# Optimization experiments

Hardware: AMD Instinct MI355X
Metric: run time of the kernel (lower is better)

## Reference

```python
import jax, jax.numpy as jnp
import numpy as np

N = 100000
E = 1600000
D_IN = 128
D_H = 128
D_OUT = 128
LN_EPS = 1e-5
NORM_EPS = 1e-12


def _sage_conv(x, src, dst, Wl, bl, Wr):
    # PyG SAGEConv(mean): out = lin_l(mean_{j in N(i)} x_j) + lin_r(x_i)
    msgs = x[src]                                             # [E, d] gather
    summed = jax.ops.segment_sum(msgs, dst, num_segments=N)   # [N, d]
    cnt = jax.ops.segment_sum(jnp.ones((src.shape[0],), x.dtype), dst, num_segments=N)
    mean = summed / jnp.maximum(cnt, 1.0)[:, None]
    return mean @ Wl + bl + x @ Wr


def _layer_norm(x, g, b):
    mu = jnp.mean(x, axis=-1, keepdims=True)
    var = jnp.mean(jnp.square(x - mu), axis=-1, keepdims=True)
    return (x - mu) * jax.lax.rsqrt(var + LN_EPS) * g + b


def setup_inputs() -> dict:
    key = jax.random.key(0)
    ks = jax.random.split(key, 20)
    x = jax.random.normal(ks[0], (N, D_IN), dtype=jnp.float32)
    edge_index = jax.random.randint(ks[1], (2, E), 0, N, dtype=jnp.int64)
    dims = [(D_IN, D_H), (D_H, D_H), (D_H, D_OUT)]
    inp = {"x": x, "edge_index": edge_index}
    for i, (di, do) in enumerate(dims):
        s = 1.0 / np.sqrt(di)
        inp[f"Wl{i}"] = jax.random.normal(ks[2 + 5 * i], (di, do), dtype=jnp.float32) * s
        inp[f"bl{i}"] = jnp.zeros((do,), dtype=jnp.float32)
        inp[f"Wr{i}"] = jax.random.normal(ks[3 + 5 * i], (di, do), dtype=jnp.float32) * s
        inp[f"g{i}"] = jnp.ones((do,), dtype=jnp.float32)
        inp[f"b{i}"] = jnp.zeros((do,), dtype=jnp.float32)
    return inp


def reference(x, edge_index, Wl0, bl0, Wr0, g0, b0, Wl1, bl1, Wr1, g1, b1, Wl2, bl2, Wr2, g2, b2):
    src, dst = edge_index[0], edge_index[1]
    params = [(Wl0, bl0, Wr0, g0, b0), (Wl1, bl1, Wr1, g1, b1), (Wl2, bl2, Wr2, g2, b2)]
    h = x
    for i, (Wl, bl, Wr, g, b) in enumerate(params):
        h = _sage_conv(h, src, dst, Wl, bl, Wr)
        h = _layer_norm(h, g, b)
        if i < len(params) - 1:
            h = jax.nn.elu(h)
            # dropout is identity in eval mode
    # F.normalize(p=2, dim=-1)
    nrm = jnp.sqrt(jnp.sum(jnp.square(h), axis=-1, keepdims=True))
    return h / jnp.maximum(nrm, NORM_EPS)
```

## Files before the change

kernel.cpp:

```cpp
#include <hip/hip_runtime.h>
#include <hip/hip_bf16.h>
#include <math.h>

#define N_NODES 100000
#define N_EDGES 1600000
#define D 128
#define NB 391
#define BSTRIDE 6000

#define OFF_SSRC 0
#define OFF_OFFS 6400000
#define OFF_PACK 6800016
#define OFF_GC   7193232
#define OFF_BB   7195296
#define OFF_M    7204112
#define OFF_XHI  58404112
#define OFF_XLO  84004112

typedef __attribute__((ext_vector_type(8))) short short8;
typedef __attribute__((ext_vector_type(4))) float floatx4;

__device__ __forceinline__ unsigned short f2bf(float f) {
    unsigned int u = __float_as_uint(f);
    u += 0x7fffu + ((u >> 16) & 1u);
    return (unsigned short)(u >> 16);
}
__device__ __forceinline__ float bf2f(unsigned short h) {
    return __uint_as_float(((unsigned int)h) << 16);
}

__global__ __launch_bounds__(256) void part_kernel(const int* __restrict__ src,
                                                   const int* __restrict__ dst,
                                                   int* __restrict__ gcur,
                                                   uint2* __restrict__ staging) {
    __shared__ int hist[NB];
    __shared__ int base[NB];
    int t = threadIdx.x;
    int e0 = blockIdx.x * 4096;
    for (int i = t; i < NB; i += 256) hist[i] = 0;
    __syncthreads();
    int d[16];
#pragma unroll
    for (int i = 0; i < 16; ++i) {
        int e = e0 + i * 256 + t;
        d[i] = (e < N_EDGES) ? dst[e] : -1;
        if (d[i] >= 0) atomicAdd(&hist[d[i] >> 8], 1);
    }
    __syncthreads();
    for (int i = t; i < NB; i += 256) {
        int h = hist[i];
        base[i] = h ? atomicAdd(&gcur[i], h) : 0;
    }
    __syncthreads();
    for (int i = t; i < NB; i += 256) hist[i] = 0;
    __syncthreads();
#pragma unroll
    for (int i = 0; i < 16; ++i) {
        if (d[i] >= 0) {
            int e = e0 + i * 256 + t;
            int b = d[i] >> 8;
            int slot = atomicAdd(&hist[b], 1);
            staging[b * BSTRIDE + base[b] + slot] =
                make_uint2((unsigned)src[e], (unsigned)(d[i] & 255));
        }
    }
}

__global__ void bscan_kernel(const int* __restrict__ gcur, int* __restrict__ bbase,
                             int* __restrict__ offs) {
    __shared__ int sh[512];
    int t = threadIdx.x;
    int v = (t < NB) ? gcur[t] : 0;
    sh[t] = v;
    __syncthreads();
    for (int off = 1; off < 512; off <<= 1) {
        int y = (t >= off) ? sh[t - off] : 0;
        __syncthreads();
        sh[t] += y;
        __syncthreads();
    }
    if (t < NB) bbase[t] = sh[t] - v;
    if (t == 0) offs[N_NODES] = N_EDGES;
}

__global__ __launch_bounds__(256) void bsort_kernel(const uint2* __restrict__ staging,
                                                    const int* __restrict__ gcur,
                                                    const int* __restrict__ bbase,
                                                    int* __restrict__ offs,
                                                    int* __restrict__ s_src) {
    __shared__ int cnt[256];
    __shared__ int scn[256];
    __shared__ int ssrc[BSTRIDE];
    int b = blockIdx.x;
    int t = threadIdx.x;
    int n = gcur[b];
    int base_out = bbase[b];
    cnt[t] = 0;
    __syncthreads();
    for (int e = t; e < n; e += 256) {
        uint2 v = staging[b * BSTRIDE + e];
        atomicAdd(&cnt[v.y], 1);
    }
    __syncthreads();
    int v = cnt[t];
    scn[t] = v;
    __syncthreads();
    for (int off = 1; off < 256; off <<= 1) {
        int y = (t >= off) ? scn[t - off] : 0;
        __syncthreads();
        scn[t] += y;
        __syncthreads();
    }
    int ex = scn[t] - v;
    int node = b * 256 + t;
    if (node < N_NODES) offs[node] = base_out + ex;
    cnt[t] = ex;
    __syncthreads();
    for (int e = t; e < n; e += 256) {
        uint2 w = staging[b * BSTRIDE + e];
        int slot = atomicAdd(&cnt[w.y], 1);
        ssrc[slot] = (int)w.x;
    }
    __syncthreads();
    for (int e = t; e < n; e += 256) s_src[base_out + e] = ssrc[e];
}

__global__ void pack_kernel(const float* __restrict__ Wl0, const float* __restrict__ Wr0,
                            const float* __restrict__ Wl1, const float* __restrict__ Wr1,
                            const float* __restrict__ Wl2, const float* __restrict__ Wr2,
                            unsigned short* __restrict__ pack) {
    int tid = blockIdx.x * blockDim.x + threadIdx.x;
    int l = tid >> 15;
    int r = tid & 32767;
    int k = r >> 7;
    int n = r & 127;
    const float* Wl = (l == 0) ? Wl0 : (l == 1) ? Wl1 : Wl2;
    const float* Wr = (l == 0) ? Wr0 : (l == 1) ? Wr1 : Wr2;
    float v = (k < 128) ? Wl[k * 128 + n] : Wr[(k - 128) * 128 + n];
    unsigned short hi = f2bf(v);
    unsigned short lo = f2bf(v - bf2f(hi));
    int ct = n >> 4, ks = k >> 5, lane = ((k >> 3) & 3) * 16 + (n & 15), j = k & 7;
    int idx = ((ct * 8 + ks) * 64 + lane) * 8 + j;
    pack[l * 65536 + idx] = hi;
    pack[l * 65536 + 32768 + idx] = lo;
}

__global__ __launch_bounds__(256) void cvt_kernel(const float* __restrict__ x,
                                                  unsigned int* __restrict__ Xhi,
                                                  unsigned int* __restrict__ Xlo) {
    int i = blockIdx.x * 256 + threadIdx.x;
    float2 v = ((const float2*)x)[i];
    unsigned short h0 = f2bf(v.x), h1 = f2bf(v.y);
    unsigned short l0 = f2bf(v.x - bf2f(h0)), l1 = f2bf(v.y - bf2f(h1));
    Xhi[i] = (unsigned int)h0 | ((unsigned int)h1 << 16);
    Xlo[i] = (unsigned int)l0 | ((unsigned int)l1 << 16);
}

__global__ __launch_bounds__(256, 5) void fused_kernel(const uint4* __restrict__ X4,
                                                       const unsigned short* __restrict__ Xh,
                                                       const unsigned short* __restrict__ Xl,
                                                       unsigned short* __restrict__ XhO,
                                                       unsigned short* __restrict__ XlO,
                                                       const int* __restrict__ s_src,
                                                       const int* __restrict__ offs,
                                                       const unsigned short* __restrict__ packh,
                                                       const unsigned short* __restrict__ packl,
                                                       const float* __restrict__ bl,
                                                       const float* __restrict__ g,
                                                       const float* __restrict__ b,
                                                       float* __restrict__ outf, int last) {
    __shared__ float lmean[64 * 128];
    int t = threadIdx.x;
    int wid = t >> 6, lane = t & 63;
    int sub = lane >> 4, li = lane & 15;
    int nodebase = blockIdx.x * 64;

    int off_l = offs[min(nodebase + wid * 16 + min(lane, 16), N_NODES)];

#define ACC_U4(u)                                                                  \
    do {                                                                           \
        const unsigned int w_[4] = {(u).x, (u).y, (u).z, (u).w};                   \
        _Pragma("unroll") for (int j_ = 0; j_ < 4; ++j_) {                         \
            acc[2 * j_]     += bf2f((unsigned short)w_[j_]);                       \
            acc[2 * j_ + 1] += bf2f((unsigned short)(w_[j_] >> 16));               \
        }                                                                          \
    } while (0)

    for (int i = 0; i < 16; ++i) {
        int lrow = wid * 16 + i;
        int beg = __shfl(off_l, i);
        int end = __shfl(off_l, i + 1);
        int deg = end - beg;
        float acc[8];
#pragma unroll
        for (int j = 0; j < 8; ++j) acc[j] = 0.f;

        for (int cbase = 0; cbase < deg; cbase += 64) {
            int cnt = min(deg - cbase, 64);
            int myidx = s_src[min(beg + cbase + lane, N_EDGES - 1)];
            int j = 0;
            for (; j + 16 <= cnt; j += 16) {
                int i0 = __shfl(myidx, j + sub);
                int i1 = __shfl(myidx, j + 4 + sub);
                int i2 = __shfl(myidx, j + 8 + sub);
                int i3 = __shfl(myidx, j + 12 + sub);
                uint4 u0 = X4[i0 * 16 + li];
                uint4 u1 = X4[i1 * 16 + li];
                uint4 u2 = X4[i2 * 16 + li];
                uint4 u3 = X4[i3 * 16 + li];
                ACC_U4(u0); ACC_U4(u1); ACC_U4(u2); ACC_U4(u3);
            }
            if (j + 8 <= cnt) {
                int i0 = __shfl(myidx, j + sub);
                int i1 = __shfl(myidx, j + 4 + sub);
                uint4 u0 = X4[i0 * 16 + li];
                uint4 u1 = X4[i1 * 16 + li];
                ACC_U4(u0); ACC_U4(u1);
                j += 8;
            }
            if (j + 4 <= cnt) {
                int i0 = __shfl(myidx, j + sub);
                uint4 u0 = X4[i0 * 16 + li];
                ACC_U4(u0);
                j += 4;
            }
            int rem = cnt - j;
            if (rem > 0) {
                int i0 = __shfl(myidx, j + min(sub, rem - 1));
                uint4 u0 = X4[i0 * 16 + li];
                if (sub < rem) ACC_U4(u0);
            }
        }
#pragma unroll
        for (int j = 0; j < 8; ++j) {
            acc[j] += __shfl_xor(acc[j], 16);
            acc[j] += __shfl_xor(acc[j], 32);
        }
        float inv = 1.0f / fmaxf((float)deg, 1.0f);
        if (sub < 2) {
            int chunk = li * 2 + sub;
            floatx4 v = {acc[sub * 4] * inv, acc[sub * 4 + 1] * inv,
                         acc[sub * 4 + 2] * inv, acc[sub * 4 + 3] * inv};
            *(floatx4*)&lmean[lrow * 128 + ((chunk ^ (lrow & 7)) << 2)] = v;
        }
    }
#undef ACC_U4

    int colb = lane & 15;
    int quad = lane >> 4;
    int kq = quad * 8;
    int tilebase = nodebase + wid * 16;

    int rowA = min(tilebase + colb, N_NODES - 1);
    int lrowA = wid * 16 + colb;
    int rsalt = lrowA & 7;

    floatx4 acc[8];
#pragma unroll
    for (int ct = 0; ct < 8; ++ct) acc[ct] = (floatx4){0.f, 0.f, 0.f, 0.f};

#pragma unroll
    for (int ks = 0; ks < 4; ++ks) {
        int chunk0 = ks * 8 + quad * 2;
        short8 ah, al;
        {
            floatx4 v0 = *(const floatx4*)&lmean[lrowA * 128 + ((chunk0 ^ rsalt) << 2)];
            floatx4 v1 = *(const floatx4*)&lmean[lrowA * 128 + (((chunk0 + 1) ^ rsalt) << 2)];
            float v[8] = {v0[0], v0[1], v0[2], v0[3], v1[0], v1[1], v1[2], v1[3]};
#pragma unroll
            for (int j = 0; j < 8; ++j) {
                unsigned short hi = f2bf(v[j]);
                ah[j] = (short)hi;
                al[j] = (short)f2bf(v[j] - bf2f(hi));
            }
        }
#pragma unroll
        for (int ct = 0; ct < 8; ++ct) {
            int fo = ((ct * 8 + ks) << 9) + (lane << 3);
            short8 bh = *(const short8*)(packh + fo);
            short8 bo = *(const short8*)(packl + fo);
            acc[ct] = __builtin_amdgcn_mfma_f32_16x16x32_bf16(ah, bh, acc[ct], 0, 0, 0);
            acc[ct] = __builtin_amdgcn_mfma_f32_16x16x32_bf16(al, bh, acc[ct], 0, 0, 0);
            acc[ct] = __builtin_amdgcn_mfma_f32_16x16x32_bf16(ah, bo, acc[ct], 0, 0, 0);
        }
    }
#pragma unroll
    for (int ks = 4; ks < 8; ++ks) {
        int kof = (ks - 4) * 32 + kq;
        long o = (long)rowA * D + kof;
        short8 ah = *(const short8*)(Xh + o);
        short8 al = *(const short8*)(Xl + o);
#pragma unroll
        for (int ct = 0; ct < 8; ++ct) {
            int fo = ((ct * 8 + ks) << 9) + (lane << 3);
            short8 bh = *(const short8*)(packh + fo);
            short8 bo = *(const short8*)(packl + fo);
            acc[ct] = __builtin_amdgcn_mfma_f32_16x16x32_bf16(ah, bh, acc[ct], 0, 0, 0);
            acc[ct] = __builtin_amdgcn_mfma_f32_16x16x32_bf16(al, bh, acc[ct], 0, 0, 0);
            acc[ct] = __builtin_amdgcn_mfma_f32_16x16x32_bf16(ah, bo, acc[ct], 0, 0, 0);
        }
    }

    float bb[8], gg[8], b2[8];
#pragma unroll
    for (int ct = 0; ct < 8; ++ct) {
        bb[ct] = bl[ct * 16 + colb];
        gg[ct] = g[ct * 16 + colb];
        b2[ct] = b[ct * 16 + colb];
    }

#pragma unroll
    for (int ct = 0; ct < 8; ++ct)
#pragma unroll
        for (int e = 0; e < 4; ++e) acc[ct][e] += bb[ct];
    float mu[4], rstd[4];
#pragma unroll
    for (int e = 0; e < 4; ++e) {
        float s = 0.f;
#pragma unroll
        for (int ct = 0; ct < 8; ++ct) s += acc[ct][e];
        s += __shfl_xor(s, 1); s += __shfl_xor(s, 2);
        s += __shfl_xor(s, 4); s += __shfl_xor(s, 8);
        mu[e] = s * (1.0f / 128.0f);
    }
#pragma unroll
    for (int e = 0; e < 4; ++e) {
        float q = 0.f;
#pragma unroll
        for (int ct = 0; ct < 8; ++ct) {
            float d = acc[ct][e] - mu[e];
            q += d * d;
        }
        q += __shfl_xor(q, 1); q += __shfl_xor(q, 2);
        q += __shfl_xor(q, 4); q += __shfl_xor(q, 8);
        rstd[e] = rsqrtf(q * (1.0f / 128.0f) + 1e-5f);
    }
#pragma unroll
    for (int ct = 0; ct < 8; ++ct)
#pragma unroll
        for (int e = 0; e < 4; ++e) {
            float y = (acc[ct][e] - mu[e]) * rstd[e] * gg[ct] + b2[ct];
            if (!last) y = (y > 0.f) ? y : expm1f(y);
            acc[ct][e] = y;
        }
    if (last) {
#pragma unroll
        for (int e = 0; e < 4; ++e) {
            float ss = 0.f;
#pragma unroll
            for (int ct = 0; ct < 8; ++ct) {
                float y = acc[ct][e];
                ss += y * y;
            }
            ss += __shfl_xor(ss, 1); ss += __shfl_xor(ss, 2);
            ss += __shfl_xor(ss, 4); ss += __shfl_xor(ss, 8);
            float inv = 1.0f / fmaxf(sqrtf(ss), 1e-12f);
#pragma unroll
            for (int ct = 0; ct < 8; ++ct) acc[ct][e] *= inv;
        }
#pragma unroll
        for (int e = 0; e < 4; ++e) {
            int row = tilebase + quad * 4 + e;
            if (row < N_NODES) {
#pragma unroll
                for (int ct = 0; ct < 8; ++ct)
                    outf[(long)row * D + ct * 16 + colb] = acc[ct][e];
            }
        }
    } else {
#pragma unroll
        for (int e = 0; e < 4; ++e) {
            int row = tilebase + quad * 4 + e;
            if (row < N_NODES) {
#pragma unroll
                for (int ct = 0; ct < 8; ++ct) {
                    float y = acc[ct][e];
                    unsigned short hh = f2bf(y);
                    unsigned short ll = f2bf(y - bf2f(hh));
                    long o = (long)row * D + ct * 16 + colb;
                    XhO[o] = hh;
                    XlO[o] = ll;
                }
            }
        }
    }
}

extern "C" void kernel_launch(void* const* d_in, const int* in_sizes, int n_in,
                              void* d_out, int out_size, void* d_ws, size_t ws_size,
                              hipStream_t stream) {
    const float* x = (const float*)d_in[0];
    const int* edges = (const int*)d_in[1];
    const int* src = edges;
    const int* dst = edges + N_EDGES;
    const float* Wl[3] = {(const float*)d_in[2], (const float*)d_in[7],  (const float*)d_in[12]};
    const float* bl[3] = {(const float*)d_in[3], (const float*)d_in[8],  (const float*)d_in[13]};
    const float* Wr[3] = {(const float*)d_in[4], (const float*)d_in[9],  (const float*)d_in[14]};
    const float* g[3]  = {(const float*)d_in[5], (const float*)d_in[10], (const float*)d_in[15]};
    const float* b[3]  = {(const float*)d_in[6], (const float*)d_in[11], (const float*)d_in[16]};

    char* ws = (char*)d_ws;
    int* s_src = (int*)(ws + OFF_SSRC);
    int* offs  = (int*)(ws + OFF_OFFS);
    unsigned short* wpack = (unsigned short*)(ws + OFF_PACK);
    int* gcur  = (int*)(ws + OFF_GC);
    int* bbase = (int*)(ws + OFF_BB);
    uint2* staging = (uint2*)(ws + OFF_M);
    unsigned short* XhB = (unsigned short*)(ws + OFF_M);
    unsigned short* XlB = (unsigned short*)(ws + OFF_M + 25600000);
    unsigned short* XhA = (unsigned short*)(ws + OFF_XHI);
    unsigned short* XlA = (unsigned short*)(ws + OFF_XLO);
    float* out = (float*)d_out;

    hipMemsetAsync(gcur, 0, NB * sizeof(int), stream);
    part_kernel<<<(N_EDGES + 4095) / 4096, 256, 0, stream>>>(src, dst, gcur, staging);
    bscan_kernel<<<1, 512, 0, stream>>>(gcur, bbase, offs);
    bsort_kernel<<<NB, 256, 0, stream>>>(staging, gcur, bbase, offs, s_src);
    pack_kernel<<<(3 * 32768) / 256, 256, 0, stream>>>(Wl[0], Wr[0], Wl[1], Wr[1], Wl[2], Wr[2], wpack);
    cvt_kernel<<<(N_NODES * 64) / 256, 256, 0, stream>>>(x, (unsigned int*)XhA, (unsigned int*)XlA);

    const int FB = (N_NODES + 63) / 64;
    unsigned short* ph[3] = {wpack, wpack + 65536, wpack + 131072};

    fused_kernel<<<FB, 256, 0, stream>>>((const uint4*)XhA, XhA, XlA, XhB, XlB,
                                         s_src, offs, ph[0], ph[0] + 32768,
                                         bl[0], g[0], b[0], nullptr, 0);
    fused_kernel<<<FB, 256, 0, stream>>>((const uint4*)XhB, XhB, XlB, XhA, XlA,
                                         s_src, offs, ph[1], ph[1] + 32768,
                                         bl[1], g[1], b[1], nullptr, 0);
    fused_kernel<<<FB, 256, 0, stream>>>((const uint4*)XhA, XhA, XlA, nullptr, nullptr,
                                         s_src, offs, ph[2], ph[2] + 32768,
                                         bl[2], g[2], b[2], out, 1);
}
```

Baseline: 592.0 us.

## Replace bucketed two-pass CSR build with global-atomic degree count and scatter

Swaps the bucket partition plus per-bucket LDS sort for a plain CSR build: global atomic degree histogram, three-stage prefix scan, then a global-atomic scatter of source indices. The degree histogram is fused into the x-to-bf16 split conversion kernel so one launch does both. It drops the staging buffer and the capacity-limited BSTRIDE buckets but relies on heavy global atomics. Neighbor order within a node becomes nondeterministic, which can change float summation order.

```diff
diff --git a/kernel.cpp b/kernel.cpp
--- a/kernel.cpp
+++ b/kernel.cpp
@@ -6,7 +6,6 @@
 #define N_EDGES 1600000
 #define D 128
 #define NB 391
-#define BSTRIDE 6000
 
 #define OFF_SSRC 0
 #define OFF_OFFS 6400000
@@ -29,48 +28,45 @@
     return __uint_as_float(((unsigned int)h) << 16);
 }
 
-__global__ __launch_bounds__(256) void part_kernel(const int* __restrict__ src,
-                                                   const int* __restrict__ dst,
-                                                   int* __restrict__ gcur,
-                                                   uint2* __restrict__ staging) {
-    __shared__ int hist[NB];
-    __shared__ int base[NB];
-    int t = threadIdx.x;
-    int e0 = blockIdx.x * 4096;
-    for (int i = t; i < NB; i += 256) hist[i] = 0;
+__global__ __launch_bounds__(256) void cvt_hist_kernel(const float* __restrict__ x,
+                                                       unsigned int* __restrict__ Xhi,
+                                                       unsigned int* __restrict__ Xlo,
+                                                       const int* __restrict__ dst,
+                                                       int* __restrict__ deg) {
+    int bid = blockIdx.x, t = threadIdx.x;
+    if (t < 64) atomicAdd(&deg[dst[bid * 64 + t]], 1);
+    int i = bid * 256 + t;
+    float2 v = ((const float2*)x)[i];
+    unsigned short h0 = f2bf(v.x), h1 = f2bf(v.y);
+    unsigned short l0 = f2bf(v.x - bf2f(h0)), l1 = f2bf(v.y - bf2f(h1));
+    Xhi[i] = (unsigned int)h0 | ((unsigned int)h1 << 16);
+    Xlo[i] = (unsigned int)l0 | ((unsigned int)l1 << 16);
+}
+
+__global__ __launch_bounds__(256) void scan1_kernel(const int* __restrict__ deg,
+                                                    int* __restrict__ offs,
+                                                    int* __restrict__ aux) {
+    __shared__ int sh[256];
+    int b = blockIdx.x, t = threadIdx.x;
+    int node = b * 256 + t;
+    int v = (node < N_NODES) ? deg[node] : 0;
+    sh[t] = v;
     __syncthreads();
-    int d[16];
-#pragma unroll
-    for (int i = 0; i < 16; ++i) {
-        int e = e0 + i * 256 + t;
-        d[i] = (e < N_EDGES) ? dst[e] : -1;
-        if (d[i] >= 0) atomicAdd(&hist[d[i] >> 8], 1);
-    }
-    __syncthreads();
-    for (int i = t; i < NB; i += 256) {
-        int h = hist[i];
-        base[i] = h ? atomicAdd(&gcur[i], h) : 0;
-    }
-    __syncthreads();
-    for (int i = t; i < NB; i += 256) hist[i] = 0;
-    __syncthreads();
-#pragma unroll
-    for (int i = 0; i < 16; ++i) {
-        if (d[i] >= 0) {
-            int e = e0 + i * 256 + t;
-            int b = d[i] >> 8;
-            int slot = atomicAdd(&hist[b], 1);
-            staging[b * BSTRIDE + base[b] + slot] =
-                make_uint2((unsigned)src[e], (unsigned)(d[i] & 255));
-        }
-    }
-}
-
-__global__ void bscan_kernel(const int* __restrict__ gcur, int* __restrict__ bbase,
+    for (int off = 1; off < 256; off <<= 1) {
+        int y = (t >= off) ? sh[t - off] : 0;
+        __syncthreads();
+        sh[t] += y;
+        __syncthreads();
+    }
+    if (node < N_NODES) offs[node] = sh[t] - v;
+    if (t == 255) aux[b] = sh[255];
+}
+
+__global__ void bscan_kernel(const int* __restrict__ aux, int* __restrict__ bbase,
                              int* __restrict__ offs) {
     __shared__ int sh[512];
     int t = threadIdx.x;
-    int v = (t < NB) ? gcur[t] : 0;
+    int v = (t < NB) ? aux[t] : 0;
     sh[t] = v;
     __syncthreads();
     for (int off = 1; off < 512; off <<= 1) {
@@ -83,46 +79,29 @@
     if (t == 0) offs[N_NODES] = N_EDGES;
 }
 
-__global__ __launch_bounds__(256) void bsort_kernel(const uint2* __restrict__ staging,
-                                                    const int* __restrict__ gcur,
-                                                    const int* __restrict__ bbase,
-                                                    int* __restrict__ offs,
-                                                    int* __restrict__ s_src) {
-    __shared__ int cnt[256];
-    __shared__ int scn[256];
-    __shared__ int ssrc[BSTRIDE];
-    int b = blockIdx.x;
+__global__ __launch_bounds__(256) void scan2_kernel(int* __restrict__ offs,
+                                                    const int* __restrict__ bbase) {
+    int b = blockIdx.x, t = threadIdx.x;
+    int node = b * 256 + t;
+    if (node < N_NODES) offs[node] += bbase[b];
+}
+
+__global__ __launch_bounds__(256) void scatter_kernel(const int* __restrict__ src,
+                                                      const int* __restrict__ dst,
+                                                      const int* __restrict__ offs,
+                                                      int* __restrict__ cnt,
+                                                      int* __restrict__ s_src) {
     int t = threadIdx.x;
-    int n = gcur[b];
-    int base_out = bbase[b];
-    cnt[t] = 0;
-    __syncthreads();
-    for (int e = t; e < n; e += 256) {
-        uint2 v = staging[b * BSTRIDE + e];
-        atomicAdd(&cnt[v.y], 1);
-    }
-    __syncthreads();
-    int v = cnt[t];
-    scn[t] = v;
-    __syncthreads();
-    for (int off = 1; off < 256; off <<= 1) {
-        int y = (t >= off) ? scn[t - off] : 0;
-        __syncthreads();
-        scn[t] += y;
-        __syncthreads();
-    }
-    int ex = scn[t] - v;
-    int node = b * 256 + t;
-    if (node < N_NODES) offs[node] = base_out + ex;
-    cnt[t] = ex;
-    __syncthreads();
-    for (int e = t; e < n; e += 256) {
-        uint2 w = staging[b * BSTRIDE + e];
-        int slot = atomicAdd(&cnt[w.y], 1);
-        ssrc[slot] = (int)w.x;
-    }
-    __syncthreads();
-    for (int e = t; e < n; e += 256) s_src[base_out + e] = ssrc[e];
+    int e0 = blockIdx.x * 4096;
+#pragma unroll
+    for (int i = 0; i < 16; ++i) {
+        int e = e0 + i * 256 + t;
+        if (e < N_EDGES) {
+            int d = dst[e];
+            int p = offs[d] + atomicAdd(&cnt[d], 1);
+            s_src[min(p, N_EDGES - 1)] = src[e];
+        }
+    }
 }
 
 __global__ void pack_kernel(const float* __restrict__ Wl0, const float* __restrict__ Wr0,
@@ -145,17 +124,6 @@
     pack[l * 65536 + 32768 + idx] = lo;
 }
 
-__global__ __launch_bounds__(256) void cvt_kernel(const float* __restrict__ x,
-                                                  unsigned int* __restrict__ Xhi,
-                                                  unsigned int* __restrict__ Xlo) {
-    int i = blockIdx.x * 256 + threadIdx.x;
-    float2 v = ((const float2*)x)[i];
-    unsigned short h0 = f2bf(v.x), h1 = f2bf(v.y);
-    unsigned short l0 = f2bf(v.x - bf2f(h0)), l1 = f2bf(v.y - bf2f(h1));
-    Xhi[i] = (unsigned int)h0 | ((unsigned int)h1 << 16);
-    Xlo[i] = (unsigned int)l0 | ((unsigned int)l1 << 16);
-}
-
 __global__ __launch_bounds__(256, 5) void fused_kernel(const uint4* __restrict__ X4,
                                                        const unsigned short* __restrict__ Xh,
                                                        const unsigned short* __restrict__ Xl,
@@ -403,21 +371,24 @@
     int* s_src = (int*)(ws + OFF_SSRC);
     int* offs  = (int*)(ws + OFF_OFFS);
     unsigned short* wpack = (unsigned short*)(ws + OFF_PACK);
-    int* gcur  = (int*)(ws + OFF_GC);
+    int* aux   = (int*)(ws + OFF_GC);
     int* bbase = (int*)(ws + OFF_BB);
-    uint2* staging = (uint2*)(ws + OFF_M);
+    int* deg   = (int*)(ws + OFF_M);
+    int* cnt   = (int*)(ws + OFF_M + 400000);
     unsigned short* XhB = (unsigned short*)(ws + OFF_M);
     unsigned short* XlB = (unsigned short*)(ws + OFF_M + 25600000);
     unsigned short* XhA = (unsigned short*)(ws + OFF_XHI);
     unsigned short* XlA = (unsigned short*)(ws + OFF_XLO);
     float* out = (float*)d_out;
 
-    hipMemsetAsync(gcur, 0, NB * sizeof(int), stream);
-    part_kernel<<<(N_EDGES + 4095) / 4096, 256, 0, stream>>>(src, dst, gcur, staging);
-    bscan_kernel<<<1, 512, 0, stream>>>(gcur, bbase, offs);
-    bsort_kernel<<<NB, 256, 0, stream>>>(staging, gcur, bbase, offs, s_src);
+    hipMemsetAsync(deg, 0, 2 * N_NODES * sizeof(int), stream);
+    cvt_hist_kernel<<<(N_NODES * 64) / 256, 256, 0, stream>>>(x, (unsigned int*)XhA,
+                                                              (unsigned int*)XlA, dst, deg);
+    scan1_kernel<<<NB, 256, 0, stream>>>(deg, offs, aux);
+    bscan_kernel<<<1, 512, 0, stream>>>(aux, bbase, offs);
+    scan2_kernel<<<NB, 256, 0, stream>>>(offs, bbase);
     pack_kernel<<<(3 * 32768) / 256, 256, 0, stream>>>(Wl[0], Wr[0], Wl[1], Wr[1], Wl[2], Wr[2], wpack);
-    cvt_kernel<<<(N_NODES * 64) / 256, 256, 0, stream>>>(x, (unsigned int*)XhA, (unsigned int*)XlA);
+    scatter_kernel<<<(N_EDGES + 4095) / 4096, 256, 0, stream>>>(src, dst, offs, cnt, s_src);
 
     const int FB = (N_NODES + 63) / 64;
     unsigned short* ph[3] = {wpack, wpack + 65536, wpack + 131072};
```

Result: slower. 681.7 us (+15.2%).
